# Optimization experiments

Hardware: AMD Instinct MI355X
Metric: run time of the kernel (lower is better)

The kernel has to match this reference:

```python
import jax, jax.numpy as jnp
import numpy as np

B, T, P, D = 4, 1024, 64, 128


def _lin_params(k, fin, fout):
    kw, kb = jax.random.split(k)
    w = jax.random.normal(kw, (fin, fout), jnp.float32) / np.sqrt(fin).astype(np.float32)
    b = jax.random.normal(kb, (fout,), jnp.float32) * 0.01
    return w, b


def setup_inputs() -> dict:
    key = jax.random.key(0)
    ks = jax.random.split(key, 10)
    positions = jax.random.normal(ks[0], (B, T, P, D), jnp.float32)
    context = jax.random.normal(ks[1], (B, T, D), jnp.float32)
    hierarchy_depth = jax.random.normal(ks[2], (B, T, P), jnp.float32)
    cw1, cb1 = _lin_params(ks[3], 2 * D, 128)
    cw2, cb2 = _lin_params(ks[4], 128, 64)
    cw3, cb3 = _lin_params(ks[5], 64, 1)
    hw1, hb1 = _lin_params(ks[6], D + 1, 32)
    hw2, hb2 = _lin_params(ks[7], 32, 16)
    hw3, hb3 = _lin_params(ks[8], 16, 1)
    curvature_memory = jnp.full((P,), -1.0, jnp.float32)  # (num_components,1) squeezed
    return {
        'positions': positions, 'context': context, 'hierarchy_depth': hierarchy_depth,
        'cw1': cw1, 'cb1': cb1, 'cw2': cw2, 'cb2': cb2, 'cw3': cw3, 'cb3': cb3,
        'hw1': hw1, 'hb1': hb1, 'hw2': hw2, 'hb2': hb2, 'hw3': hw3, 'hb3': hb3,
        'curvature_memory': curvature_memory,
    }


def _local_curvatures(positions):
    # positions: (B,T,P,D) -> flatten point clouds
    pf = positions.reshape(-1, P, D)                      # (BT,P,D)
    sq = jnp.sum(pf * pf, axis=-1)                        # (BT,P)
    d2 = sq[:, :, None] + sq[:, None, :] - 2.0 * jnp.einsum('npd,nqd->npq', pf, pf)
    dist = jnp.sqrt(jnp.maximum(d2, 1e-12))               # (BT,P,P), cdist
    k = min(3, P - 1)
    # k+1 smallest distances (includes self distance ~0 at slot 0)
    neg_small, _ = jax.lax.top_k(-dist, k + 1)            # (BT,P,k+1)
    nearest = -neg_small                                  # ascending
    mean_dist = nearest[:, :, 1:].mean(axis=-1)
    density = 1.0 / (mean_dist + 1e-6)
    curv = -2.0 * jnp.tanh(density)
    return curv.reshape(B, T, P)


def reference(positions, context, hierarchy_depth,
              cw1, cb1, cw2, cb2, cw3, cb3,
              hw1, hb1, hw2, hb2, hw3, hb3,
              curvature_memory):
    local = _local_curvatures(positions)                  # (B,T,P)

    # context encoder: cat(pos, ctx) -> 128 relu -> 64 relu -> 1
    ctx_exp = jnp.broadcast_to(context[:, :, None, :], (B, T, P, D))
    ci = jnp.concatenate([positions, ctx_exp], axis=-1)   # (B,T,P,2D)
    h = jax.nn.relu(ci @ cw1 + cb1)
    h = jax.nn.relu(h @ cw2 + cb2)
    ctx_curv = (h @ cw3 + cb3)[..., 0]                    # (B,T,P)

    # hierarchy net: cat(pos, tanh(depth)) -> 32 relu -> 16 tanh -> 1
    hi = jnp.concatenate([positions, jnp.tanh(hierarchy_depth)[..., None]], axis=-1)
    g = jax.nn.relu(hi @ hw1 + hb1)
    g = jnp.tanh(g @ hw2 + hb2)
    hier_curv = (g @ hw3 + hb3)[..., 0]                   # (B,T,P)

    combined = 0.5 * local + 0.3 * ctx_curv + 0.2 * hier_curv

    # momentum memory update + smoothing (momentum=0.9, adaptation_rate=0.1)
    cur_mean = combined.mean(axis=(0, 1))                 # (P,)
    new_mem = 0.9 * curvature_memory + 0.1 * cur_mean
    smoothed = 0.9 * combined + 0.1 * new_mem[None, None, :]
    return jnp.clip(smoothed, -5.0, 2.0)
```

## Files before the change

kernel.cpp:

```cpp
#include <hip/hip_runtime.h>
#include <hip/hip_bf16.h>

typedef __attribute__((ext_vector_type(4))) float  float4v;
typedef __attribute__((ext_vector_type(2))) unsigned int uint2v;
typedef __attribute__((ext_vector_type(8))) short  short8v;
typedef __attribute__((ext_vector_type(4))) float  f32x4;

__device__ __forceinline__ unsigned short f2bf(float f) {
    unsigned int u = __float_as_uint(f);
    u += 0x7FFFu + ((u >> 16) & 1u);
    return (unsigned short)(u >> 16);
}

__device__ __forceinline__ int swzb(int row, int kbyte) {
    return row * 256 + (kbyte ^ ((row & 7) << 4));
}
__device__ __forceinline__ int swzh(int row, int kbyte) {
    return row * 256 + (kbyte ^ ((row & 7) << 4) ^ ((row & 8) << 2));
}

__global__ void prep_weights(const float* __restrict__ cw1, const float* __restrict__ cw2,
                             const float* __restrict__ hw1, const float* __restrict__ hw2,
                             unsigned short* __restrict__ w1bT, unsigned short* __restrict__ w2bT,
                             unsigned short* __restrict__ hw1T, unsigned short* __restrict__ hw2T) {
    int i = blockIdx.x * 256 + threadIdx.x;
    if (i < 16384) {
        int j = i >> 7, k = i & 127;
        w1bT[i] = f2bf(cw1[k * 128 + j]);
    } else if (i < 24576) {
        int t = i - 16384; int j = t >> 7, k = t & 127;
        w2bT[t] = f2bf(cw2[k * 64 + j]);
    } else if (i < 28672) {
        int t = i - 24576; int j = t >> 7, k = t & 127;
        hw1T[t] = f2bf(hw1[k * 32 + j]);
    } else if (i < 29184) {
        int t = i - 28672; int j = t >> 5, k = t & 31;
        hw2T[t] = f2bf(hw2[k * 16 + j]);
    }
}

__global__ __launch_bounds__(256) void ctx_gemm(const float* __restrict__ ctx,
                                                const float* __restrict__ cw1,
                                                const float* __restrict__ cb1,
                                                float* __restrict__ ctxW1) {
    __shared__ float ldsW[128 * 128];
    __shared__ float ldsC[16 * 128];
    const int tid = threadIdx.x;
    const int bt0 = blockIdx.x * 16;
    for (int i = tid; i < 16384; i += 256) {
        int d = i >> 7, j = i & 127;
        ldsW[i] = cw1[(128 + d) * 128 + j];
    }
    for (int i = tid; i < 2048; i += 256) ldsC[i] = ctx[bt0 * 128 + i];
    __syncthreads();
    const int j = tid & 127, half = tid >> 7;
    float acc[8];
    float bj = cb1[j];
#pragma unroll
    for (int k = 0; k < 8; ++k) acc[k] = bj;
    for (int d = 0; d < 128; ++d) {
        float wv = ldsW[d * 128 + j];
#pragma unroll
        for (int k = 0; k < 8; ++k) acc[k] += ldsC[(half * 8 + k) * 128 + d] * wv;
    }
#pragma unroll
    for (int k = 0; k < 8; ++k) ctxW1[(size_t)(bt0 + half * 8 + k) * 128 + j] = acc[k];
}

__global__ __launch_bounds__(256, 4) void fused_main(
    const float* __restrict__ pos_g, const float* __restrict__ dep_g,
    const float* __restrict__ cb2,  const float* __restrict__ cw3,
    const float* __restrict__ cb3,  const float* __restrict__ hw1,
    const float* __restrict__ hb1,  const float* __restrict__ hb2,
    const float* __restrict__ hw3,  const float* __restrict__ hb3,
    const unsigned short* __restrict__ w1bT, const unsigned short* __restrict__ w2bT,
    const unsigned short* __restrict__ hw1T, const unsigned short* __restrict__ hw2T,
    const float* __restrict__ ctxW1g, float* __restrict__ out)
{
    __shared__ __align__(16) short posB[64 * 128];
    __shared__ __align__(16) short h1B[64 * 128];
    __shared__ __align__(16) short g1B[64 * 32];
    __shared__ float tdep[64], diag[64], localc[64], hierc[64];
    __shared__ float ctxp[256];

    const int bt  = blockIdx.x;
    const int tid = threadIdx.x;
    const int lane = tid & 63;
    const int w   = tid >> 6;
    const int lr  = lane & 15;
    const int lk  = lane >> 4;
    const int R   = w * 16;

    const short8v* w1p8 = (const short8v*)w1bT;
    const short8v* w2p8 = (const short8v*)w2bT;
    short8v w1f[2][4], w2f[4];
#pragma unroll
    for (int jtl = 0; jtl < 2; ++jtl)
#pragma unroll
        for (int ks = 0; ks < 4; ++ks)
            w1f[jtl][ks] = w1p8[(32 * w + jtl * 16 + lr) * 16 + ks * 4 + lk];
#pragma unroll
    for (int ks = 0; ks < 4; ++ks)
        w2f[ks] = w2p8[(16 * w + lr) * 16 + ks * 4 + lk];
    short8v hw2f = ((const short8v*)hw2T)[lr * 4 + lk];
    float cvals[2];
    cvals[0] = ctxW1g[(size_t)bt * 128 + 32 * w + lr];
    cvals[1] = ctxW1g[(size_t)bt * 128 + 32 * w + 16 + lr];
    float cb2v = cb2[16 * w + lr], cw3v = cw3[16 * w + lr], cb3v = cb3[0];
    float hb2v = hb2[lr], hw3v = hw3[lr], hb3v = hb3[0];

    const float4v* pos4 = (const float4v*)(pos_g + (size_t)bt * 8192);
#pragma unroll
    for (int i = 0; i < 8; ++i) {
        int c = tid + 256 * i;
        int row = c >> 5, c4 = c & 31;
        float4v v = pos4[c];
        __hip_bfloat162 lo2 = __float22bfloat162_rn(make_float2(v[0], v[1]));
        __hip_bfloat162 hi2 = __float22bfloat162_rn(make_float2(v[2], v[3]));
        unsigned int u0, u1;
        __builtin_memcpy(&u0, &lo2, 4);
        __builtin_memcpy(&u1, &hi2, 4);
        uint2v uu = {u0, u1};
        *(uint2v*)((char*)posB + row * 256 + ((c4 * 8) ^ ((row & 7) << 4))) = uu;
    }
    if (tid < 64) tdep[tid] = tanhf(dep_g[bt * 64 + tid]);
    __syncthreads();

    f32x4 g0 = {0.f,0.f,0.f,0.f}, g1t = {0.f,0.f,0.f,0.f},
          g2t = {0.f,0.f,0.f,0.f}, g3t = {0.f,0.f,0.f,0.f};
#pragma unroll
    for (int ks = 0; ks < 4; ++ks) {
        int kb = ks * 64 + lk * 16;
        short8v a = *(const short8v*)((const char*)posB + swzb(R + lr, kb));
        short8v b0 = *(const short8v*)((const char*)posB + swzb(0  + lr, kb));
        short8v b1 = *(const short8v*)((const char*)posB + swzb(16 + lr, kb));
        short8v b2 = *(const short8v*)((const char*)posB + swzb(32 + lr, kb));
        short8v b3 = *(const short8v*)((const char*)posB + swzb(48 + lr, kb));
        g0 = __builtin_amdgcn_mfma_f32_16x16x32_bf16(a, b0, g0, 0, 0, 0);
        g1t = __builtin_amdgcn_mfma_f32_16x16x32_bf16(a, b1, g1t, 0, 0, 0);
        g2t = __builtin_amdgcn_mfma_f32_16x16x32_bf16(a, b2, g2t, 0, 0, 0);
        g3t = __builtin_amdgcn_mfma_f32_16x16x32_bf16(a, b3, g3t, 0, 0, 0);
    }
    {
        f32x4 gw = (w == 0) ? g0 : (w == 1) ? g1t : (w == 2) ? g2t : g3t;
        int e = lr & 3;
        float dv = (e == 0) ? gw[0] : (e == 1) ? gw[1] : (e == 2) ? gw[2] : gw[3];
        if (lk == (lr >> 2)) diag[R + lr] = dv;
    }
    __syncthreads();

    {
        float s0[4], s1[4], s2[4], s3[4];
#pragma unroll
        for (int e = 0; e < 4; ++e) {
            int p = R + 4 * lk + e;
            float dp = diag[p];
            s0[e] = s1[e] = s2[e] = s3[e] = 1e30f;
#pragma unroll
            for (int jt = 0; jt < 4; ++jt) {
                f32x4 gt = (jt == 0) ? g0 : (jt == 1) ? g1t : (jt == 2) ? g2t : g3t;
                float gv = (e == 0) ? gt[0] : (e == 1) ? gt[1] : (e == 2) ? gt[2] : gt[3];
                float d2 = dp + diag[jt * 16 + lr] - 2.f * gv;
                float c0 = fminf(s0[e], d2), m0 = fmaxf(s0[e], d2);
                float c1 = fminf(s1[e], m0), m1 = fmaxf(s1[e], m0);
                float c2 = fminf(s2[e], m1), m2 = fmaxf(s2[e], m1);
                float c3 = fminf(s3[e], m2);
                s0[e] = c0; s1[e] = c1; s2[e] = c2; s3[e] = c3;
            }
        }
#pragma unroll
        for (int m = 1; m <= 8; m <<= 1) {
#pragma unroll
            for (int e = 0; e < 4; ++e) {
                float t0 = __shfl_xor(s0[e], m);
                float t1 = __shfl_xor(s1[e], m);
                float t2 = __shfl_xor(s2[e], m);
                float t3 = __shfl_xor(s3[e], m);
                float r0 = fminf(s0[e], t3), r1 = fminf(s1[e], t2);
                float r2 = fminf(s2[e], t1), r3 = fminf(s3[e], t0);
                float a0 = fminf(r0, r2), b0 = fmaxf(r0, r2);
                float a1 = fminf(r1, r3), b1 = fmaxf(r1, r3);
                s0[e] = fminf(a0, a1); s1[e] = fmaxf(a0, a1);
                s2[e] = fminf(b0, b1); s3[e] = fmaxf(b0, b1);
            }
        }
        if (lr == 0) {
#pragma unroll
            for (int e = 0; e < 4; ++e) {
                float d1 = sqrtf(fmaxf(s1[e], 1e-12f));
                float d2 = sqrtf(fmaxf(s2[e], 1e-12f));
                float d3 = sqrtf(fmaxf(s3[e], 1e-12f));
                float mean = (d1 + d2 + d3) * (1.f / 3.f);
                localc[R + 4 * lk + e] = -2.f * tanhf(1.f / (mean + 1e-6f));
            }
        }
    }

    {
        f32x4 h1a[4][2];
#pragma unroll
        for (int rt = 0; rt < 4; ++rt)
#pragma unroll
            for (int jtl = 0; jtl < 2; ++jtl) h1a[rt][jtl] = (f32x4){0.f,0.f,0.f,0.f};
#pragma unroll
        for (int ks = 0; ks < 4; ++ks) {
            int kb = ks * 64 + lk * 16;
#pragma unroll
            for (int rt = 0; rt < 4; ++rt) {
                short8v a = *(const short8v*)((const char*)posB + swzb(rt * 16 + lr, kb));
                h1a[rt][0] = __builtin_amdgcn_mfma_f32_16x16x32_bf16(a, w1f[0][ks], h1a[rt][0], 0, 0, 0);
                h1a[rt][1] = __builtin_amdgcn_mfma_f32_16x16x32_bf16(a, w1f[1][ks], h1a[rt][1], 0, 0, 0);
            }
        }
#pragma unroll
        for (int rt = 0; rt < 4; ++rt)
#pragma unroll
            for (int jtl = 0; jtl < 2; ++jtl) {
                int j = 32 * w + jtl * 16 + lr;
                float add = cvals[jtl];
#pragma unroll
                for (int e = 0; e < 4; ++e) {
                    int p = rt * 16 + 4 * lk + e;
                    float v = fmaxf(h1a[rt][jtl][e] + add, 0.f);
                    *(short*)((char*)h1B + swzh(p, 2 * j)) = (short)f2bf(v);
                }
            }
    }
    __syncthreads();

    const short8v* hw1p8 = (const short8v*)hw1T;
    short8v hw1f[2][4];
#pragma unroll
    for (int jt = 0; jt < 2; ++jt)
#pragma unroll
        for (int ks = 0; ks < 4; ++ks)
            hw1f[jt][ks] = hw1p8[(jt * 16 + lr) * 16 + ks * 4 + lk];
    float u1v[2], hb1v[2];
#pragma unroll
    for (int jt = 0; jt < 2; ++jt) { u1v[jt] = hw1[4096 + jt * 16 + lr]; hb1v[jt] = hb1[jt * 16 + lr]; }
    {
        f32x4 h2[4];
#pragma unroll
        for (int rt = 0; rt < 4; ++rt) h2[rt] = (f32x4){0.f,0.f,0.f,0.f};
#pragma unroll
        for (int ks = 0; ks < 4; ++ks) {
            int kb = ks * 64 + lk * 16;
#pragma unroll
            for (int rt = 0; rt < 4; ++rt) {
                short8v a = *(const short8v*)((const char*)h1B + swzh(rt * 16 + lr, kb));
                h2[rt] = __builtin_amdgcn_mfma_f32_16x16x32_bf16(a, w2f[ks], h2[rt], 0, 0, 0);
            }
        }
        float s4[4][4];
#pragma unroll
        for (int rt = 0; rt < 4; ++rt)
#pragma unroll
            for (int e = 0; e < 4; ++e)
                s4[rt][e] = fmaxf(h2[rt][e] + cb2v, 0.f) * cw3v;
#pragma unroll
        for (int m = 1; m <= 8; m <<= 1) {
#pragma unroll
            for (int rt = 0; rt < 4; ++rt)
#pragma unroll
                for (int e = 0; e < 4; ++e) s4[rt][e] += __shfl_xor(s4[rt][e], m);
        }
        if (lr == 0) {
#pragma unroll
            for (int rt = 0; rt < 4; ++rt)
#pragma unroll
                for (int e = 0; e < 4; ++e)
                    ctxp[w * 64 + rt * 16 + 4 * lk + e] = s4[rt][e];
        }
    }

    {
        f32x4 q0 = {0.f,0.f,0.f,0.f}, q1 = {0.f,0.f,0.f,0.f};
#pragma unroll
        for (int ks = 0; ks < 4; ++ks) {
            int kb = ks * 64 + lk * 16;
            short8v a = *(const short8v*)((const char*)posB + swzb(R + lr, kb));
            q0 = __builtin_amdgcn_mfma_f32_16x16x32_bf16(a, hw1f[0][ks], q0, 0, 0, 0);
            q1 = __builtin_amdgcn_mfma_f32_16x16x32_bf16(a, hw1f[1][ks], q1, 0, 0, 0);
        }
#pragma unroll
        for (int jt = 0; jt < 2; ++jt) {
            int j = jt * 16 + lr;
#pragma unroll
            for (int e = 0; e < 4; ++e) {
                int p = R + 4 * lk + e;
                f32x4 qq = (jt == 0) ? q0 : q1;
                float v = fmaxf(qq[e] + tdep[p] * u1v[jt] + hb1v[jt], 0.f);
                *(short*)((char*)g1B + p * 64 + ((2 * j) ^ ((p & 3) << 4))) = (short)f2bf(v);
            }
        }
    }
    asm volatile("s_waitcnt lgkmcnt(0)" ::: "memory");

    {
        int p2 = R + lr;
        short8v a = *(const short8v*)((const char*)g1B + p2 * 64 + ((lk * 16) ^ ((p2 & 3) << 4)));
        f32x4 g2 = {0.f,0.f,0.f,0.f};
        g2 = __builtin_amdgcn_mfma_f32_16x16x32_bf16(a, hw2f, g2, 0, 0, 0);
        float sh[4];
#pragma unroll
        for (int e = 0; e < 4; ++e) sh[e] = tanhf(g2[e] + hb2v) * hw3v;
#pragma unroll
        for (int m = 1; m <= 8; m <<= 1) {
#pragma unroll
            for (int e = 0; e < 4; ++e) sh[e] += __shfl_xor(sh[e], m);
        }
        if (lr == 0) {
#pragma unroll
            for (int e = 0; e < 4; ++e) hierc[R + 4 * lk + e] = sh[e] + hb3v;
        }
    }
    __syncthreads();

    if (tid < 64) {
        float ctxv = ctxp[tid] + ctxp[64 + tid] + ctxp[128 + tid] + ctxp[192 + tid] + cb3v;
        float comb = 0.5f * localc[tid] + 0.3f * ctxv + 0.2f * hierc[tid];
        out[(size_t)bt * 64 + tid] = comb;
    }
}

__global__ void reduce1(const float* __restrict__ comb, float* __restrict__ partials) {
    __shared__ float sm[256];
    int b = blockIdx.x, tid = threadIdx.x;
    const float* src = comb + (size_t)b * 1024;
    float s = 0.f;
#pragma unroll
    for (int k = 0; k < 4; ++k) s += src[tid + 256 * k];
    sm[tid] = s;
    __syncthreads();
    if (tid < 64) partials[b * 64 + tid] = sm[tid] + sm[tid + 64] + sm[tid + 128] + sm[tid + 192];
}

__global__ void reduce2(const float* __restrict__ partials, const float* __restrict__ mem,
                        float* __restrict__ newmem) {
    int p = threadIdx.x;
    float s0 = 0.f, s1 = 0.f, s2 = 0.f, s3 = 0.f;
    for (int b = 0; b < 256; b += 4) {
        s0 += partials[(b + 0) * 64 + p];
        s1 += partials[(b + 1) * 64 + p];
        s2 += partials[(b + 2) * 64 + p];
        s3 += partials[(b + 3) * 64 + p];
    }
    float s = (s0 + s1) + (s2 + s3);
    newmem[p] = 0.9f * mem[p] + 0.1f * (s * (1.f / 4096.f));
}

__global__ void finalize(float* __restrict__ out, const float* __restrict__ newmem) {
    int t = blockIdx.x * 256 + threadIdx.x;
    float4v v = *(float4v*)(out + 4 * (size_t)t);
    float4v nm = *(const float4v*)(newmem + ((4 * t) & 63));
#pragma unroll
    for (int e = 0; e < 4; ++e) {
        float x = 0.9f * v[e] + 0.1f * nm[e];
        v[e] = fminf(fmaxf(x, -5.f), 2.f);
    }
    *(float4v*)(out + 4 * (size_t)t) = v;
}

extern "C" void kernel_launch(void* const* d_in, const int* in_sizes, int n_in,
                              void* d_out, int out_size, void* d_ws, size_t ws_size,
                              hipStream_t stream) {
    (void)in_sizes; (void)n_in; (void)out_size; (void)ws_size;
    const float* pos = (const float*)d_in[0];
    const float* ctx = (const float*)d_in[1];
    const float* dep = (const float*)d_in[2];
    const float* cw1 = (const float*)d_in[3];
    const float* cb1 = (const float*)d_in[4];
    const float* cw2 = (const float*)d_in[5];
    const float* cb2 = (const float*)d_in[6];
    const float* cw3 = (const float*)d_in[7];
    const float* cb3 = (const float*)d_in[8];
    const float* hw1 = (const float*)d_in[9];
    const float* hb1 = (const float*)d_in[10];
    const float* hw2 = (const float*)d_in[11];
    const float* hb2 = (const float*)d_in[12];
    const float* hw3 = (const float*)d_in[13];
    const float* hb3 = (const float*)d_in[14];
    const float* cmem = (const float*)d_in[15];
    float* out = (float*)d_out;
    float* ws = (float*)d_ws;
    float* partials = ws;
    float* newmem = ws + 16384;
    unsigned short* wT = (unsigned short*)(ws + 16448);
    unsigned short* w1bT = wT;
    unsigned short* w2bT = wT + 16384;
    unsigned short* hw1T = wT + 24576;
    unsigned short* hw2T = wT + 28672;
    float* ctxW1 = ws + 31040;

    prep_weights<<<114, 256, 0, stream>>>(cw1, cw2, hw1, hw2, w1bT, w2bT, hw1T, hw2T);
    ctx_gemm<<<256, 256, 0, stream>>>(ctx, cw1, cb1, ctxW1);
    fused_main<<<4096, 256, 0, stream>>>(pos, dep, cb2, cw3, cb3,
                                         hw1, hb1, hb2, hw3, hb3,
                                         w1bT, w2bT, hw1T, hw2T, ctxW1, out);
    reduce1<<<256, 256, 0, stream>>>(out, partials);
    reduce2<<<1, 64, 0, stream>>>(partials, cmem, newmem);
    finalize<<<256, 256, 0, stream>>>(out, newmem);
}
```

Baseline: 86.45 us.

## Merge prep kernels, add fast tanh/rcp, MFMA priority, packed stores, parallel reduce2

Merges the weight-conversion and context GEMM kernels into one launch. Replaces tanhf/sqrtf/division with exp2-based tanh and hardware rcp/sqrt intrinsics, and defers the per-row diagonal add until after top-k selection. Adds s_setprio around the MFMA loops, packs bf16 conversions in pairs, simplifies the pos-load addressing, and widens reduce2 to 256 threads with an LDS reduction. The fast math intrinsics lose a little accuracy.

```diff
diff --git a/kernel.cpp b/kernel.cpp
--- a/kernel.cpp
+++ b/kernel.cpp
@@ -12,6 +12,12 @@
     return (unsigned short)(u >> 16);
 }
 
+__device__ __forceinline__ float ftanh(float x) {
+    float s = fminf(x * 2.8853900817779268f, 115.0f);
+    float t = exp2f(s);
+    return (t - 1.0f) * __builtin_amdgcn_rcpf(t + 1.0f);
+}
+
 __device__ __forceinline__ int swzb(int row, int kbyte) {
     return row * 256 + (kbyte ^ ((row & 7) << 4));
 }
@@ -19,52 +25,52 @@
     return row * 256 + (kbyte ^ ((row & 7) << 4) ^ ((row & 8) << 2));
 }
 
-__global__ void prep_weights(const float* __restrict__ cw1, const float* __restrict__ cw2,
-                             const float* __restrict__ hw1, const float* __restrict__ hw2,
-                             unsigned short* __restrict__ w1bT, unsigned short* __restrict__ w2bT,
-                             unsigned short* __restrict__ hw1T, unsigned short* __restrict__ hw2T) {
-    int i = blockIdx.x * 256 + threadIdx.x;
-    if (i < 16384) {
-        int j = i >> 7, k = i & 127;
-        w1bT[i] = f2bf(cw1[k * 128 + j]);
-    } else if (i < 24576) {
-        int t = i - 16384; int j = t >> 7, k = t & 127;
-        w2bT[t] = f2bf(cw2[k * 64 + j]);
-    } else if (i < 28672) {
-        int t = i - 24576; int j = t >> 7, k = t & 127;
-        hw1T[t] = f2bf(hw1[k * 32 + j]);
-    } else if (i < 29184) {
-        int t = i - 28672; int j = t >> 5, k = t & 31;
-        hw2T[t] = f2bf(hw2[k * 16 + j]);
-    }
-}
-
-__global__ __launch_bounds__(256) void ctx_gemm(const float* __restrict__ ctx,
-                                                const float* __restrict__ cw1,
-                                                const float* __restrict__ cb1,
-                                                float* __restrict__ ctxW1) {
+__global__ __launch_bounds__(256) void prep_all(
+    const float* __restrict__ ctx,  const float* __restrict__ cw1,
+    const float* __restrict__ cb1,  const float* __restrict__ cw2,
+    const float* __restrict__ hw1,  const float* __restrict__ hw2,
+    unsigned short* __restrict__ w1bT, unsigned short* __restrict__ w2bT,
+    unsigned short* __restrict__ hw1T, unsigned short* __restrict__ hw2T,
+    float* __restrict__ ctxW1) {
     __shared__ float ldsW[128 * 128];
     __shared__ float ldsC[16 * 128];
     const int tid = threadIdx.x;
-    const int bt0 = blockIdx.x * 16;
-    for (int i = tid; i < 16384; i += 256) {
-        int d = i >> 7, j = i & 127;
-        ldsW[i] = cw1[(128 + d) * 128 + j];
-    }
-    for (int i = tid; i < 2048; i += 256) ldsC[i] = ctx[bt0 * 128 + i];
-    __syncthreads();
-    const int j = tid & 127, half = tid >> 7;
-    float acc[8];
-    float bj = cb1[j];
-#pragma unroll
-    for (int k = 0; k < 8; ++k) acc[k] = bj;
-    for (int d = 0; d < 128; ++d) {
-        float wv = ldsW[d * 128 + j];
-#pragma unroll
-        for (int k = 0; k < 8; ++k) acc[k] += ldsC[(half * 8 + k) * 128 + d] * wv;
-    }
-#pragma unroll
-    for (int k = 0; k < 8; ++k) ctxW1[(size_t)(bt0 + half * 8 + k) * 128 + j] = acc[k];
+    if (blockIdx.x < 256) {
+        const int bt0 = blockIdx.x * 16;
+        for (int i = tid; i < 16384; i += 256) {
+            int d = i >> 7, j = i & 127;
+            ldsW[i] = cw1[(128 + d) * 128 + j];
+        }
+        for (int i = tid; i < 2048; i += 256) ldsC[i] = ctx[bt0 * 128 + i];
+        __syncthreads();
+        const int j = tid & 127, half = tid >> 7;
+        float acc[8];
+        float bj = cb1[j];
+#pragma unroll
+        for (int k = 0; k < 8; ++k) acc[k] = bj;
+        for (int d = 0; d < 128; ++d) {
+            float wv = ldsW[d * 128 + j];
+#pragma unroll
+            for (int k = 0; k < 8; ++k) acc[k] += ldsC[(half * 8 + k) * 128 + d] * wv;
+        }
+#pragma unroll
+        for (int k = 0; k < 8; ++k) ctxW1[(size_t)(bt0 + half * 8 + k) * 128 + j] = acc[k];
+    } else {
+        int i = (blockIdx.x - 256) * 256 + tid;
+        if (i < 16384) {
+            int j = i >> 7, k = i & 127;
+            w1bT[i] = f2bf(cw1[k * 128 + j]);
+        } else if (i < 24576) {
+            int t = i - 16384; int j = t >> 7, k = t & 127;
+            w2bT[t] = f2bf(cw2[k * 64 + j]);
+        } else if (i < 28672) {
+            int t = i - 24576; int j = t >> 7, k = t & 127;
+            hw1T[t] = f2bf(hw1[k * 32 + j]);
+        } else if (i < 29184) {
+            int t = i - 28672; int j = t >> 5, k = t & 31;
+            hw2T[t] = f2bf(hw2[k * 16 + j]);
+        }
+    }
 }
 
 __global__ __launch_bounds__(256, 4) void fused_main(
@@ -109,25 +115,28 @@
     float cb2v = cb2[16 * w + lr], cw3v = cw3[16 * w + lr], cb3v = cb3[0];
     float hb2v = hb2[lr], hw3v = hw3[lr], hb3v = hb3[0];
 
-    const float4v* pos4 = (const float4v*)(pos_g + (size_t)bt * 8192);
-#pragma unroll
-    for (int i = 0; i < 8; ++i) {
-        int c = tid + 256 * i;
-        int row = c >> 5, c4 = c & 31;
-        float4v v = pos4[c];
-        __hip_bfloat162 lo2 = __float22bfloat162_rn(make_float2(v[0], v[1]));
-        __hip_bfloat162 hi2 = __float22bfloat162_rn(make_float2(v[2], v[3]));
-        unsigned int u0, u1;
-        __builtin_memcpy(&u0, &lo2, 4);
-        __builtin_memcpy(&u1, &hi2, 4);
-        uint2v uu = {u0, u1};
-        *(uint2v*)((char*)posB + row * 256 + ((c4 * 8) ^ ((row & 7) << 4))) = uu;
-    }
-    if (tid < 64) tdep[tid] = tanhf(dep_g[bt * 64 + tid]);
+    {
+        const float4v* gp = (const float4v*)(pos_g + (size_t)bt * 8192) + tid;
+        const int srow = tid >> 5, sc4 = tid & 31;
+        char* lp = (char*)posB + srow * 256 + ((sc4 * 8) ^ ((srow & 7) << 4));
+#pragma unroll
+        for (int i = 0; i < 8; ++i) {
+            float4v v = gp[256 * i];
+            __hip_bfloat162 lo2 = __float22bfloat162_rn(make_float2(v[0], v[1]));
+            __hip_bfloat162 hi2 = __float22bfloat162_rn(make_float2(v[2], v[3]));
+            unsigned int u0, u1;
+            __builtin_memcpy(&u0, &lo2, 4);
+            __builtin_memcpy(&u1, &hi2, 4);
+            uint2v uu = {u0, u1};
+            *(uint2v*)(lp + 2048 * i) = uu;
+        }
+    }
+    if (tid < 64) tdep[tid] = ftanh(dep_g[bt * 64 + tid]);
     __syncthreads();
 
     f32x4 g0 = {0.f,0.f,0.f,0.f}, g1t = {0.f,0.f,0.f,0.f},
           g2t = {0.f,0.f,0.f,0.f}, g3t = {0.f,0.f,0.f,0.f};
+    __builtin_amdgcn_s_setprio(1);
 #pragma unroll
     for (int ks = 0; ks < 4; ++ks) {
         int kb = ks * 64 + lk * 16;
@@ -141,6 +150,7 @@
         g2t = __builtin_amdgcn_mfma_f32_16x16x32_bf16(a, b2, g2t, 0, 0, 0);
         g3t = __builtin_amdgcn_mfma_f32_16x16x32_bf16(a, b3, g3t, 0, 0, 0);
     }
+    __builtin_amdgcn_s_setprio(0);
     {
         f32x4 gw = (w == 0) ? g0 : (w == 1) ? g1t : (w == 2) ? g2t : g3t;
         int e = lr & 3;
@@ -153,14 +163,12 @@
         float s0[4], s1[4], s2[4], s3[4];
 #pragma unroll
         for (int e = 0; e < 4; ++e) {
-            int p = R + 4 * lk + e;
-            float dp = diag[p];
             s0[e] = s1[e] = s2[e] = s3[e] = 1e30f;
 #pragma unroll
             for (int jt = 0; jt < 4; ++jt) {
                 f32x4 gt = (jt == 0) ? g0 : (jt == 1) ? g1t : (jt == 2) ? g2t : g3t;
                 float gv = (e == 0) ? gt[0] : (e == 1) ? gt[1] : (e == 2) ? gt[2] : gt[3];
-                float d2 = dp + diag[jt * 16 + lr] - 2.f * gv;
+                float d2 = diag[jt * 16 + lr] - 2.f * gv;
                 float c0 = fminf(s0[e], d2), m0 = fmaxf(s0[e], d2);
                 float c1 = fminf(s1[e], m0), m1 = fmaxf(s1[e], m0);
                 float c2 = fminf(s2[e], m1), m2 = fmaxf(s2[e], m1);
@@ -187,11 +195,12 @@
         if (lr == 0) {
 #pragma unroll
             for (int e = 0; e < 4; ++e) {
-                float d1 = sqrtf(fmaxf(s1[e], 1e-12f));
-                float d2 = sqrtf(fmaxf(s2[e], 1e-12f));
-                float d3 = sqrtf(fmaxf(s3[e], 1e-12f));
+                float dp = diag[R + 4 * lk + e];
+                float d1 = __builtin_amdgcn_sqrtf(fmaxf(dp + s1[e], 1e-12f));
+                float d2 = __builtin_amdgcn_sqrtf(fmaxf(dp + s2[e], 1e-12f));
+                float d3 = __builtin_amdgcn_sqrtf(fmaxf(dp + s3[e], 1e-12f));
                 float mean = (d1 + d2 + d3) * (1.f / 3.f);
-                localc[R + 4 * lk + e] = -2.f * tanhf(1.f / (mean + 1e-6f));
+                localc[R + 4 * lk + e] = -2.f * ftanh(__builtin_amdgcn_rcpf(mean + 1e-6f));
             }
         }
     }
@@ -202,6 +211,7 @@
         for (int rt = 0; rt < 4; ++rt)
 #pragma unroll
             for (int jtl = 0; jtl < 2; ++jtl) h1a[rt][jtl] = (f32x4){0.f,0.f,0.f,0.f};
+        __builtin_amdgcn_s_setprio(1);
 #pragma unroll
         for (int ks = 0; ks < 4; ++ks) {
             int kb = ks * 64 + lk * 16;
@@ -212,6 +222,7 @@
                 h1a[rt][1] = __builtin_amdgcn_mfma_f32_16x16x32_bf16(a, w1f[1][ks], h1a[rt][1], 0, 0, 0);
             }
         }
+        __builtin_amdgcn_s_setprio(0);
 #pragma unroll
         for (int rt = 0; rt < 4; ++rt)
 #pragma unroll
@@ -219,10 +230,15 @@
                 int j = 32 * w + jtl * 16 + lr;
                 float add = cvals[jtl];
 #pragma unroll
-                for (int e = 0; e < 4; ++e) {
-                    int p = rt * 16 + 4 * lk + e;
-                    float v = fmaxf(h1a[rt][jtl][e] + add, 0.f);
-                    *(short*)((char*)h1B + swzh(p, 2 * j)) = (short)f2bf(v);
+                for (int ep = 0; ep < 4; ep += 2) {
+                    float v0 = fmaxf(h1a[rt][jtl][ep] + add, 0.f);
+                    float v1 = fmaxf(h1a[rt][jtl][ep + 1] + add, 0.f);
+                    __hip_bfloat162 pk = __float22bfloat162_rn(make_float2(v0, v1));
+                    unsigned int u;
+                    __builtin_memcpy(&u, &pk, 4);
+                    int p0 = rt * 16 + 4 * lk + ep;
+                    *(unsigned short*)((char*)h1B + swzh(p0, 2 * j)) = (unsigned short)u;
+                    *(unsigned short*)((char*)h1B + swzh(p0 + 1, 2 * j)) = (unsigned short)(u >> 16);
                 }
             }
     }
@@ -242,6 +258,7 @@
         f32x4 h2[4];
 #pragma unroll
         for (int rt = 0; rt < 4; ++rt) h2[rt] = (f32x4){0.f,0.f,0.f,0.f};
+        __builtin_amdgcn_s_setprio(1);
 #pragma unroll
         for (int ks = 0; ks < 4; ++ks) {
             int kb = ks * 64 + lk * 16;
@@ -251,6 +268,7 @@
                 h2[rt] = __builtin_amdgcn_mfma_f32_16x16x32_bf16(a, w2f[ks], h2[rt], 0, 0, 0);
             }
         }
+        __builtin_amdgcn_s_setprio(0);
         float s4[4][4];
 #pragma unroll
         for (int rt = 0; rt < 4; ++rt)
@@ -285,12 +303,18 @@
 #pragma unroll
         for (int jt = 0; jt < 2; ++jt) {
             int j = jt * 16 + lr;
-#pragma unroll
-            for (int e = 0; e < 4; ++e) {
-                int p = R + 4 * lk + e;
-                f32x4 qq = (jt == 0) ? q0 : q1;
-                float v = fmaxf(qq[e] + tdep[p] * u1v[jt] + hb1v[jt], 0.f);
-                *(short*)((char*)g1B + p * 64 + ((2 * j) ^ ((p & 3) << 4))) = (short)f2bf(v);
+            float uj = u1v[jt], bj = hb1v[jt];
+            f32x4 qq = (jt == 0) ? q0 : q1;
+#pragma unroll
+            for (int ep = 0; ep < 4; ep += 2) {
+                int p0 = R + 4 * lk + ep;
+                float v0 = fmaxf(qq[ep] + tdep[p0] * uj + bj, 0.f);
+                float v1 = fmaxf(qq[ep + 1] + tdep[p0 + 1] * uj + bj, 0.f);
+                __hip_bfloat162 pk = __float22bfloat162_rn(make_float2(v0, v1));
+                unsigned int u;
+                __builtin_memcpy(&u, &pk, 4);
+                *(unsigned short*)((char*)g1B + p0 * 64 + ((2 * j) ^ ((p0 & 3) << 4))) = (unsigned short)u;
+                *(unsigned short*)((char*)g1B + (p0 + 1) * 64 + ((2 * j) ^ (((p0 + 1) & 3) << 4))) = (unsigned short)(u >> 16);
             }
         }
     }
@@ -303,7 +327,7 @@
         g2 = __builtin_amdgcn_mfma_f32_16x16x32_bf16(a, hw2f, g2, 0, 0, 0);
         float sh[4];
 #pragma unroll
-        for (int e = 0; e < 4; ++e) sh[e] = tanhf(g2[e] + hb2v) * hw3v;
+        for (int e = 0; e < 4; ++e) sh[e] = ftanh(g2[e] + hb2v) * hw3v;
 #pragma unroll
         for (int m = 1; m <= 8; m <<= 1) {
 #pragma unroll
@@ -337,16 +361,17 @@
 
 __global__ void reduce2(const float* __restrict__ partials, const float* __restrict__ mem,
                         float* __restrict__ newmem) {
-    int p = threadIdx.x;
-    float s0 = 0.f, s1 = 0.f, s2 = 0.f, s3 = 0.f;
-    for (int b = 0; b < 256; b += 4) {
-        s0 += partials[(b + 0) * 64 + p];
-        s1 += partials[(b + 1) * 64 + p];
-        s2 += partials[(b + 2) * 64 + p];
-        s3 += partials[(b + 3) * 64 + p];
-    }
-    float s = (s0 + s1) + (s2 + s3);
-    newmem[p] = 0.9f * mem[p] + 0.1f * (s * (1.f / 4096.f));
+    __shared__ float sm[256];
+    int tid = threadIdx.x;
+    int p = tid & 63, grp = tid >> 6;
+    float s = 0.f;
+    for (int b = grp; b < 256; b += 4) s += partials[b * 64 + p];
+    sm[tid] = s;
+    __syncthreads();
+    if (tid < 64) {
+        float t = sm[tid] + sm[tid + 64] + sm[tid + 128] + sm[tid + 192];
+        newmem[tid] = 0.9f * mem[tid] + 0.1f * (t * (1.f / 4096.f));
+    }
 }
 
 __global__ void finalize(float* __restrict__ out, const float* __restrict__ newmem) {
@@ -392,12 +417,12 @@
     unsigned short* hw2T = wT + 28672;
     float* ctxW1 = ws + 31040;
 
-    prep_weights<<<114, 256, 0, stream>>>(cw1, cw2, hw1, hw2, w1bT, w2bT, hw1T, hw2T);
-    ctx_gemm<<<256, 256, 0, stream>>>(ctx, cw1, cb1, ctxW1);
+    prep_all<<<370, 256, 0, stream>>>(ctx, cw1, cb1, cw2, hw1, hw2,
+                                      w1bT, w2bT, hw1T, hw2T, ctxW1);
     fused_main<<<4096, 256, 0, stream>>>(pos, dep, cb2, cw3, cb3,
                                          hw1, hb1, hb2, hw3, hb3,
                                          w1bT, w2bT, hw1T, hw2T, ctxW1, out);
     reduce1<<<256, 256, 0, stream>>>(out, partials);
-    reduce2<<<1, 64, 0, stream>>>(partials, cmem, newmem);
+    reduce2<<<1, 256, 0, stream>>>(partials, cmem, newmem);
     finalize<<<256, 256, 0, stream>>>(out, newmem);
 }
```

Measured after the change: 90.75 us. 5.0% more time.
